# Kernel tuning notes

Hardware: AMD Instinct MI355X
Metric: run time of the kernel (lower is better)

The kernel has to match this reference:

```python
import jax, jax.numpy as jnp
import numpy as np

BATCH, N_NODES, FEAT = 32, 511, 512
N_EDGES = N_NODES - 1
N_ITERS = 9  # balanced binary tree height + 1


def setup_inputs():
    key = jax.random.key(0)
    ks = jax.random.split(key, 10)
    # balanced binary tree: node p has children 2p+1, 2p+2; leaves get order 0
    depth = np.floor(np.log2(np.arange(N_NODES) + 1)).astype(np.int32)
    order = (N_ITERS - 1 - depth).astype(np.int32)
    parents = np.repeat(np.arange((N_NODES - 1) // 2), 2).astype(np.int32)
    children = np.arange(1, N_NODES, dtype=np.int32)
    adj = np.stack([children, parents], axis=1)  # rows: [child, parent]
    eorder = order[parents]
    start = np.arange(N_NODES, dtype=np.int32)
    end = np.minimum(start + 3, N_NODES - 1).astype(np.int32)
    fin = np.stack([start, end], axis=1)
    tile = lambda a: jnp.tile(jnp.asarray(a)[None], (BATCH,) + (1,) * a.ndim)
    s = 1.0 / np.sqrt(FEAT)
    s2 = 1.0 / np.sqrt(2 * FEAT)
    return dict(
        features=jax.random.normal(ks[0], (BATCH, N_NODES, FEAT), jnp.float32),
        node_order=tile(order),
        adjacency_list=tile(adj),
        edge_order=tile(eorder),
        finlist=tile(fin),
        eh=jax.random.normal(ks[1], (BATCH, 2 * FEAT), jnp.float32),
        W_learnnode=jax.random.normal(ks[2], (FEAT, 2 * FEAT), jnp.float32) * s2,
        W_learntype_forw=jax.random.normal(ks[3], (FEAT, 2 * FEAT), jnp.float32) * s2,
        W_U_iou=jax.random.normal(ks[4], (3 * FEAT, FEAT), jnp.float32) * s,
        W_U_fe_iou=jax.random.normal(ks[5], (3 * FEAT, FEAT), jnp.float32) * s,
        b_U_fe_iou=jax.random.normal(ks[6], (3 * FEAT,), jnp.float32) * 0.01,
        W_U_f=jax.random.normal(ks[7], (FEAT, FEAT), jnp.float32) * s,
        W_U_fe_f=jax.random.normal(ks[8], (FEAT, FEAT), jnp.float32) * s,
        b_U_fe_f=jax.random.normal(ks[9], (FEAT,), jnp.float32) * 0.01,
    )


def _tree(feat, node_order, adj, edge_order, finlist, e_node, e_forw,
          W_U_iou, W_U_fe_iou, b_U_fe_iou, W_U_f, W_U_fe_f, b_U_fe_f):
    N, F = feat.shape
    j = jnp.arange(N)
    # ---- getfeature: attention-pool feature spans against e_node ----
    start, end = finlist[:, 0], finlist[:, 1]
    valid = start >= 0
    span = (j[None, :] >= start[:, None]) & (j[None, :] <= end[:, None])
    span = span | (~valid[:, None] & (j[None, :] == 0))  # keep softmax finite for dead rows
    scores = feat @ e_node  # [N]
    probs = jax.nn.softmax(jnp.where(span, scores[None, :], -jnp.inf), axis=-1)
    feat2 = jnp.where(valid[:, None], probs @ feat, 0.0)  # trainmyfeature
    numofnode = valid.sum()
    # ---- level-synchronous child-sum TreeLSTM ----
    child, parent = adj[:, 0], adj[:, 1]
    fe_iou = feat2 @ W_U_fe_iou.T + b_U_fe_iou          # U_fe_iou(features), all nodes
    fe_f = feat2[parent] @ W_U_fe_f.T + b_U_fe_f        # U_fe_f(features[parent]), all edges
    h = jnp.zeros((N, F), feat.dtype)
    c = jnp.zeros((N, F), feat.dtype)
    for n in range(N_ITERS):
        nm = (node_order == n)[:, None]
        if n == 0:
            iou = fe_iou
            c_sum = 0.0
        else:
            em = (edge_order == n).astype(feat.dtype)[:, None]
            ch, cc = h[child], c[child]
            h_sum = jnp.zeros((N, F), feat.dtype).at[parent].add(ch * em)
            iou = h_sum @ W_U_iou.T + fe_iou
            f = jax.nn.sigmoid(ch @ W_U_f.T + fe_f)
            c_sum = jnp.zeros((N, F), feat.dtype).at[parent].add(f * cc * em)
        i_g, o_g, u_g = jnp.split(iou, 3, axis=1)
        c_new = jax.nn.sigmoid(i_g) * jax.nn.relu(u_g) + c_sum
        h_new = jax.nn.sigmoid(o_g) * jnp.tanh(c_new)
        c = jnp.where(nm, c_new, c)
        h = jnp.where(nm, h_new, h)
    # ---- getfinalout: attention-pool h[0:numofnode] against e_forw ----
    root_mask = j < numofnode
    s = jax.nn.softmax(jnp.where(root_mask, (h * e_forw).sum(-1), -jnp.inf))
    return (s[:, None] * h).sum(0)


def reference(features, node_order, adjacency_list, edge_order, finlist, eh,
              W_learnnode, W_learntype_forw, W_U_iou, W_U_fe_iou, b_U_fe_iou,
              W_U_f, W_U_fe_f, b_U_fe_f):
    e_node = eh @ W_learnnode.T          # learnnode(eh)
    e_forw = eh @ W_learntype_forw.T     # learntype_forw(eh)
    return jax.vmap(_tree, in_axes=(0,) * 7 + (None,) * 6)(
        features, node_order, adjacency_list, edge_order, finlist, e_node, e_forw,
        W_U_iou, W_U_fe_iou, b_U_fe_iou, W_U_f, W_U_fe_f, b_U_fe_f)
```

## Files before the change

### kernel.cpp

```cpp
#include <hip/hip_runtime.h>
#include <hip/hip_bf16.h>

#define BATCH 32
#define NN 511
#define FEAT 512
#define NFEAT ((long)32*NN*FEAT)

typedef _Float16 half8 __attribute__((ext_vector_type(8)));
typedef float f32x4 __attribute__((ext_vector_type(4)));

__device__ __forceinline__ float bf2f(unsigned short u){
  union { unsigned int i; float f; } v; v.i = ((unsigned int)u) << 16; return v.f;
}
__device__ __forceinline__ float sigm(float x){ return 1.0f/(1.0f+expf(-x)); }
__device__ __forceinline__ float ldf(const void* p, long i, int f32){
  return f32 ? ((const float*)p)[i] : bf2f(((const unsigned short*)p)[i]);
}
__device__ __forceinline__ void gload_lds16(const _Float16* g, _Float16* l){
  __builtin_amdgcn_global_load_lds(
      (const __attribute__((address_space(1))) unsigned int*)g,
      (__attribute__((address_space(3))) unsigned int*)l, 16, 0, 0);
}

__global__ void detect_kernel(const unsigned short* __restrict__ p, int* __restrict__ flag){
  __shared__ int cnt;
  if (threadIdx.x == 0) cnt = 0;
  __syncthreads();
  int local = 0;
  for (int i = threadIdx.x; i < 4096; i += 256){
    unsigned short u = p[2*i];
    int e = (u >> 7) & 0xFF;
    if (u != 0 && e >= 117 && e <= 133) local++;
  }
  atomicAdd(&cnt, local);
  __syncthreads();
  if (threadIdx.x == 0) *flag = (cnt > 2048) ? 0 : 1;
}

__global__ void cvt_all(
    const void* __restrict__ feat, const void* __restrict__ Wiou,
    const void* __restrict__ Wfeiou, const void* __restrict__ Wf,
    const void* __restrict__ Wfef, const void* __restrict__ eh,
    const void* __restrict__ Wln, const void* __restrict__ Wlf,
    const void* __restrict__ biou, const void* __restrict__ bfv,
    _Float16* __restrict__ feat_h, _Float16* __restrict__ Wiou_h,
    _Float16* __restrict__ Wfeiou_h, _Float16* __restrict__ Wf_h,
    _Float16* __restrict__ Wfef_h, _Float16* __restrict__ eh_h,
    _Float16* __restrict__ Wln_h, _Float16* __restrict__ Wlf_h,
    float* __restrict__ biou_f, float* __restrict__ bf_f,
    const int* __restrict__ flag)
{
  long g = ((long)blockIdx.x*256 + threadIdx.x)*8;
  int f32 = *flag;
  const long S1 = NFEAT;
  const long S2 = S1 + 786432;
  const long S3 = S2 + 786432;
  const long S4 = S3 + 262144;
  const long S5 = S4 + 262144;
  const long S6 = S5 + 32768;
  const long S7 = S6 + 524288;
  const long S8 = S7 + 524288;
  const long S9 = S8 + 1536;
  const long SA = S9 + 512;
  if (g >= SA) return;
  if (g >= S9){
    long o = g - S9;
    for (int q = 0; q < 8; q++) bf_f[o+q] = ldf(bfv, o+q, f32);
    return;
  }
  if (g >= S8){
    long o = g - S8;
    for (int q = 0; q < 8; q++) biou_f[o+q] = ldf(biou, o+q, f32);
    return;
  }
  const void* src; _Float16* dst; long off;
  if      (g < S1){ src=feat;   dst=feat_h;   off=g; }
  else if (g < S2){ src=Wiou;   dst=Wiou_h;   off=g-S1; }
  else if (g < S3){ src=Wfeiou; dst=Wfeiou_h; off=g-S2; }
  else if (g < S4){ src=Wf;     dst=Wf_h;     off=g-S3; }
  else if (g < S5){ src=Wfef;   dst=Wfef_h;   off=g-S4; }
  else if (g < S6){ src=eh;     dst=eh_h;     off=g-S5; }
  else if (g < S7){ src=Wln;    dst=Wln_h;    off=g-S6; }
  else            { src=Wlf;    dst=Wlf_h;    off=g-S7; }
  #pragma unroll
  for (int q = 0; q < 8; q++) dst[off+q] = (_Float16)ldf(src, off+q, f32);
}

__global__ __launch_bounds__(64) void e_mfma(
    const _Float16* __restrict__ eh,
    const _Float16* __restrict__ Wn,
    const _Float16* __restrict__ Wf,
    float* __restrict__ e_node, float* __restrict__ e_forw)
{
  int lane = threadIdx.x;
  int m = lane & 15, quad = lane >> 4;
  int n = blockIdx.x*16 + m;
  const _Float16* wrow = (n < 512) ? (Wn + (long)n*1024) : (Wf + (long)(n-512)*1024);
  f32x4 acc[2] = {};
  for (int ks = 0; ks < 32; ks++){
    int kk = ks*32 + quad*8;
    half8 bfr = *(const half8*)(wrow + kk);
    #pragma unroll
    for (int i = 0; i < 2; i++){
      half8 afr = *(const half8*)(eh + (long)(i*16 + m)*1024 + kk);
      acc[i] = __builtin_amdgcn_mfma_f32_16x16x32_f16(afr, bfr, acc[i], 0, 0, 0);
    }
  }
  float* dst = (n < 512) ? e_node : e_forw;
  int col = (n < 512) ? n : (n - 512);
  #pragma unroll
  for (int i = 0; i < 2; i++)
    #pragma unroll
    for (int reg = 0; reg < 4; reg++){
      int b = i*16 + quad*4 + reg;
      dst[b*FEAT + col] = acc[i][reg];
    }
}

__global__ __launch_bounds__(64) void feat2_kernel(
    const _Float16* __restrict__ feat,
    const int* __restrict__ finlist,
    const float* __restrict__ e_node,
    _Float16* __restrict__ feat2){
  int i = blockIdx.x, b = blockIdx.y, lane = threadIdx.x;
  int s0 = finlist[(b*NN+i)*2+0];
  int e0 = finlist[(b*NN+i)*2+1];
  s0 = min(max(s0, 0), NN-1);
  e0 = min(max(e0, s0), NN-1);
  int w = min(e0 - s0 + 1, 4);

  const _Float16* base = feat + ((long)b*NN + s0)*FEAT + lane*8;
  half8 v[4];
  #pragma unroll
  for (int q = 0; q < 4; q++){
    if (q < w) v[q] = *(const half8*)(base + (long)q*FEAT);
    else       v[q] = half8{};
  }
  const float* ep = e_node + b*FEAT + lane*8;
  f32x4 ev0 = *(const f32x4*)ep;
  f32x4 ev1 = *(const f32x4*)(ep+4);
  float en[8] = {ev0[0],ev0[1],ev0[2],ev0[3],ev1[0],ev1[1],ev1[2],ev1[3]};

  float s[4];
  #pragma unroll
  for (int q = 0; q < 4; q++){
    float acc = 0.f;
    #pragma unroll
    for (int j = 0; j < 8; j++) acc += (float)v[q][j]*en[j];
    s[q] = acc;
  }
  #pragma unroll
  for (int q = 0; q < 4; q++)
    #pragma unroll
    for (int off = 1; off < 64; off <<= 1)
      s[q] += __shfl_xor(s[q], off, 64);

  float mx = -1e30f;
  #pragma unroll
  for (int q = 0; q < 4; q++){
    if (q >= w) s[q] = -1e30f;
    mx = fmaxf(mx, s[q]);
  }
  float p[4]; float den = 0.f;
  #pragma unroll
  for (int q = 0; q < 4; q++){ p[q] = (q < w) ? expf(s[q]-mx) : 0.f; den += p[q]; }
  float inv = 1.f/den;

  half8 o;
  #pragma unroll
  for (int j = 0; j < 8; j++){
    float acc = 0.f;
    #pragma unroll
    for (int q = 0; q < 4; q++) acc += p[q]*(float)v[q][j];
    o[j] = (_Float16)(acc*inv);
  }
  *(half8*)(feat2 + ((long)b*NN + i)*FEAT + lane*8) = o;
}

__global__ __launch_bounds__(256) void fe_gemm(
    const _Float16* __restrict__ feat2,
    const _Float16* __restrict__ Wfeiou, const _Float16* __restrict__ Wfef,
    const float* __restrict__ biou, const float* __restrict__ bf,
    _Float16* __restrict__ fe_iou, _Float16* __restrict__ fe_f)
{
  __shared__ _Float16 Abuf[2][128*64];
  __shared__ _Float16 Bbuf[2][64*64];
  const int MT = 32*NN;
  int tid = threadIdx.x;
  int wv = tid >> 6, lane = tid & 63;
  int m = lane & 15, quad = lane >> 4;
  int cg = blockIdx.y;
  int rowbase = blockIdx.x*128;
  int which = (cg < 24) ? 0 : 1;
  int colbase = which ? (cg-24)*64 : cg*64;
  const _Float16* W = which ? Wfef : Wfeiou;

  const _Float16* gA[4];
  {
    #pragma unroll
    for (int t = 0; t < 4; t++){
      int c = wv*64 + lane + t*256;
      int rt = c >> 3, kc = c & 7;
      int r = rowbase + rt; if (r >= MT) r = MT - 1;
      int bb = r / NN, node = r - bb*NN;
      int srcn = which ? ((node >= 1) ? ((node-1)>>1) : 0) : node;
      gA[t] = feat2 + ((long)bb*NN + srcn)*FEAT + ((kc ^ (rt & 7))<<3);
    }
  }
  const _Float16* gB[2];
  {
    #pragma unroll
    for (int t = 0; t < 2; t++){
      int c = wv*64 + lane + t*256;
      int rt = c >> 3, kc = c & 7;
      gB[t] = W + (long)(colbase + rt)*FEAT + ((kc ^ (rt & 7))<<3);
    }
  }

  int aoff[2][2], boff[4][2];
  #pragma unroll
  for (int i = 0; i < 2; i++)
    #pragma unroll
    for (int ks = 0; ks < 2; ks++){
      int rt = wv*32 + i*16 + m;
      aoff[i][ks] = rt*128 + (((ks*4 + quad) ^ (rt & 7))<<4);
    }
  #pragma unroll
  for (int j = 0; j < 4; j++)
    #pragma unroll
    for (int ks = 0; ks < 2; ks++){
      int rt = j*16 + m;
      boff[j][ks] = rt*128 + (((ks*4 + quad) ^ (rt & 7))<<4);
    }

  f32x4 acc[2][4] = {};

  #pragma unroll
  for (int t = 0; t < 4; t++)
    gload_lds16(gA[t], &Abuf[0][(wv*64 + t*256)*8]);
  #pragma unroll
  for (int t = 0; t < 2; t++)
    gload_lds16(gB[t], &Bbuf[0][(wv*64 + t*256)*8]);

  for (int it = 0; it < 8; ++it){
    int cur = it & 1;
    __syncthreads();
    if (it < 7){
      int kk = (it+1)*64;
      #pragma unroll
      for (int t = 0; t < 4; t++)
        gload_lds16(gA[t] + kk, &Abuf[cur^1][(wv*64 + t*256)*8]);
      #pragma unroll
      for (int t = 0; t < 2; t++)
        gload_lds16(gB[t] + kk, &Bbuf[cur^1][(wv*64 + t*256)*8]);
    }
    const char* Ab_ = (const char*)&Abuf[cur][0];
    const char* Bb_ = (const char*)&Bbuf[cur][0];
    #pragma unroll
    for (int ks = 0; ks < 2; ks++){
      half8 a0 = *(const half8*)(Ab_ + aoff[0][ks]);
      half8 a1 = *(const half8*)(Ab_ + aoff[1][ks]);
      #pragma unroll
      for (int j = 0; j < 4; j++){
        half8 bfr = *(const half8*)(Bb_ + boff[j][ks]);
        acc[0][j] = __builtin_amdgcn_mfma_f32_16x16x32_f16(a0, bfr, acc[0][j], 0, 0, 0);
        acc[1][j] = __builtin_amdgcn_mfma_f32_16x16x32_f16(a1, bfr, acc[1][j], 0, 0, 0);
      }
    }
  }
  __syncthreads();

  const float* bias = which ? bf : biou;
  float bs[4];
  #pragma unroll
  for (int j = 0; j < 4; j++) bs[j] = bias[colbase + j*16 + m];

  _Float16* sl = &Abuf[0][wv*16*72];
  int lr = lane >> 2;
  int lc = (lane & 3) * 16;
  #pragma unroll
  for (int i = 0; i < 2; i++){
    #pragma unroll
    for (int j = 0; j < 4; j++)
      #pragma unroll
      for (int reg = 0; reg < 4; reg++)
        sl[(quad*4+reg)*72 + j*16 + m] = (_Float16)(acc[i][j][reg] + bs[j]);
    half8 o0 = *(const half8*)&sl[lr*72 + lc];
    half8 o1 = *(const half8*)&sl[lr*72 + lc + 8];
    int r = rowbase + wv*32 + i*16 + lr;
    if (r < MT){
      int b = r / NN, node = r - b*NN;
      if (which == 0){
        _Float16* dst = fe_iou + ((long)b*NN + node)*1536 + colbase + lc;
        *(half8*)dst = o0; *(half8*)(dst+8) = o1;
      } else if (node >= 1){
        _Float16* dst = fe_f + ((long)b*NN + node)*FEAT + colbase + lc;
        *(half8*)dst = o0; *(half8*)(dst+8) = o1;
      }
    }
  }
}

__global__ __launch_bounds__(256) void gemm_level_staged(
    int P, int lp,
    const _Float16* __restrict__ hbuf, const _Float16* __restrict__ hsum,
    const _Float16* __restrict__ Wiou, const _Float16* __restrict__ Wf,
    _Float16* __restrict__ fe_iou, _Float16* __restrict__ fe_f)
{
  __shared__ _Float16 Abuf[2][128*64];
  __shared__ _Float16 Bbuf[2][64*64];
  int Mtot = P << 5;
  int tid = threadIdx.x;
  int wv = tid >> 6, lane = tid & 63;
  int m = lane & 15, quad = lane >> 4;
  int cg = blockIdx.y;
  int rowbase = blockIdx.x*128;
  int p0 = P - 1, c0 = 2*P - 1;
  int which, colbase;
  if (cg < 24)      { which = 0; colbase = cg*64; }
  else if (cg < 32) { which = 1; colbase = (cg-24)*64; }
  else              { which = 2; colbase = (cg-32)*64; }
  const _Float16* W = (which == 0) ? Wiou : Wf;

  const _Float16* gA[4];
  {
    #pragma unroll
    for (int t = 0; t < 4; t++){
      int c = wv*64 + lane + t*256;
      int rt = c >> 3, kc = c & 7;
      int r = rowbase + rt; if (r >= Mtot) r = Mtot - 1;
      int bb = r >> lp, p = r & (P-1);
      const _Float16* base;
      if (which == 0) base = hsum + ((long)bb*128 + p)*FEAT;
      else            base = hbuf + ((long)bb*NN + c0 + 2*p + (which==2))*FEAT;
      gA[t] = base + ((kc ^ (rt & 7))<<3);
    }
  }
  const _Float16* gB[2];
  {
    #pragma unroll
    for (int t = 0; t < 2; t++){
      int c = wv*64 + lane + t*256;
      int rt = c >> 3, kc = c & 7;
      gB[t] = W + (long)(colbase + rt)*FEAT + ((kc ^ (rt & 7))<<3);
    }
  }

  int aoff[2][2], boff[4][2];
  #pragma unroll
  for (int i = 0; i < 2; i++)
    #pragma unroll
    for (int ks = 0; ks < 2; ks++){
      int rt = wv*32 + i*16 + m;
      aoff[i][ks] = rt*128 + (((ks*4 + quad) ^ (rt & 7))<<4);
    }
  #pragma unroll
  for (int j = 0; j < 4; j++)
    #pragma unroll
    for (int ks = 0; ks < 2; ks++){
      int rt = j*16 + m;
      boff[j][ks] = rt*128 + (((ks*4 + quad) ^ (rt & 7))<<4);
    }

  f32x4 acc[2][4] = {};

  #pragma unroll
  for (int t = 0; t < 4; t++)
    gload_lds16(gA[t], &Abuf[0][(wv*64 + t*256)*8]);
  #pragma unroll
  for (int t = 0; t < 2; t++)
    gload_lds16(gB[t], &Bbuf[0][(wv*64 + t*256)*8]);

  for (int it = 0; it < 8; ++it){
    int cur = it & 1;
    __syncthreads();
    if (it < 7){
      int kk = (it+1)*64;
      #pragma unroll
      for (int t = 0; t < 4; t++)
        gload_lds16(gA[t] + kk, &Abuf[cur^1][(wv*64 + t*256)*8]);
      #pragma unroll
      for (int t = 0; t < 2; t++)
        gload_lds16(gB[t] + kk, &Bbuf[cur^1][(wv*64 + t*256)*8]);
    }
    const char* Ab_ = (const char*)&Abuf[cur][0];
    const char* Bb_ = (const char*)&Bbuf[cur][0];
    #pragma unroll
    for (int ks = 0; ks < 2; ks++){
      half8 a0 = *(const half8*)(Ab_ + aoff[0][ks]);
      half8 a1 = *(const half8*)(Ab_ + aoff[1][ks]);
      #pragma unroll
      for (int j = 0; j < 4; j++){
        half8 bfr = *(const half8*)(Bb_ + boff[j][ks]);
        acc[0][j] = __builtin_amdgcn_mfma_f32_16x16x32_f16(a0, bfr, acc[0][j], 0, 0, 0);
        acc[1][j] = __builtin_amdgcn_mfma_f32_16x16x32_f16(a1, bfr, acc[1][j], 0, 0, 0);
      }
    }
  }
  __syncthreads();

  float* fsl = (float*)((char*)&Abuf[0][0] + wv*(16*68*4));
  int lr = lane >> 2;
  int lc = (lane & 3) * 16;
  #pragma unroll
  for (int i = 0; i < 2; i++){
    #pragma unroll
    for (int j = 0; j < 4; j++)
      #pragma unroll
      for (int reg = 0; reg < 4; reg++)
        fsl[(quad*4+reg)*68 + j*16 + m] = acc[i][j][reg];
    f32x4 a0 = *(const f32x4*)&fsl[lr*68 + lc];
    f32x4 a1 = *(const f32x4*)&fsl[lr*68 + lc + 4];
    f32x4 a2 = *(const f32x4*)&fsl[lr*68 + lc + 8];
    f32x4 a3 = *(const f32x4*)&fsl[lr*68 + lc + 12];
    int r = rowbase + wv*32 + i*16 + lr;
    if (r < Mtot){
      int b = r >> lp, p = r & (P-1);
      _Float16* dst;
      if (which == 0) dst = fe_iou + ((long)b*NN + p0 + p)*1536 + colbase + lc;
      else            dst = fe_f  + ((long)b*NN + c0 + 2*p + (which-1))*FEAT + colbase + lc;
      half8 f0 = *(const half8*)dst;
      half8 f1 = *(const half8*)(dst+8);
      half8 o0, o1;
      #pragma unroll
      for (int q = 0; q < 4; q++){
        o0[q]   = (_Float16)(a0[q] + (float)f0[q]);
        o0[q+4] = (_Float16)(a1[q] + (float)f0[q+4]);
        o1[q]   = (_Float16)(a2[q] + (float)f1[q]);
        o1[q+4] = (_Float16)(a3[q] + (float)f1[q+4]);
      }
      *(half8*)dst = o0; *(half8*)(dst+8) = o1;
    }
  }
}

__global__ __launch_bounds__(64) void gemm_level_h(
    int P, int lp,
    const _Float16* __restrict__ hbuf,
    const _Float16* __restrict__ Wiou, const _Float16* __restrict__ Wf,
    _Float16* __restrict__ fe_iou, _Float16* __restrict__ fe_f)
{
  __shared__ float ldsf[16*64];
  int lane = threadIdx.x;
  int m = lane & 15, quad = lane >> 4;
  int cg = blockIdx.y;
  int Mtot = P << 5;
  int rowbase = blockIdx.x*64;
  if (rowbase >= Mtot) return;
  int p0 = P - 1, c0 = 2*P - 1;

  int which, colbase;
  if (cg < 24)      { which = 0; colbase = cg*64; }
  else if (cg < 32) { which = 1; colbase = (cg-24)*64; }
  else              { which = 2; colbase = (cg-32)*64; }

  const _Float16* W = (which == 0) ? Wiou : Wf;
  bool dual = (which == 0);

  f32x4 acc[4][4] = {};
  const _Float16* ap[4];
  const _Float16* wp[4];
  #pragma unroll
  for (int i = 0; i < 4; i++){
    int r = rowbase + i*16 + m;
    if (r >= Mtot) r = Mtot - 1;
    int b = r >> lp, p = r & (P-1);
    int node = c0 + 2*p + ((which == 2) ? 1 : 0);
    ap[i] = hbuf + ((long)b*NN + node)*FEAT + quad*8;
    wp[i] = W + (long)(colbase + i*16 + m)*FEAT + quad*8;
  }

  half8 Ab[3][4], A2b[3][4], Bb[3][4];
  #pragma unroll
  for (int s = 0; s < 2; s++){
    long kk = (long)s*32;
    #pragma unroll
    for (int i = 0; i < 4; i++){
      Ab[s][i] = *(const half8*)(ap[i] + kk);
      if (dual) A2b[s][i] = *(const half8*)(ap[i] + FEAT + kk);
      Bb[s][i] = *(const half8*)(wp[i] + kk);
    }
  }
  #pragma unroll
  for (int ks = 0; ks < 16; ++ks){
    int cur = ks % 3;
    if (ks + 2 < 16){
      int nxt = (ks + 2) % 3;
      long kk = (long)(ks + 2)*32;
      #pragma unroll
      for (int i = 0; i < 4; i++){
        Ab[nxt][i] = *(const half8*)(ap[i] + kk);
        if (dual) A2b[nxt][i] = *(const half8*)(ap[i] + FEAT + kk);
        Bb[nxt][i] = *(const half8*)(wp[i] + kk);
      }
    }
    half8 av[4];
    #pragma unroll
    for (int i = 0; i < 4; i++){
      av[i] = Ab[cur][i];
      if (dual) av[i] = av[i] + A2b[cur][i];
    }
    #pragma unroll
    for (int i = 0; i < 4; i++)
      #pragma unroll
      for (int j = 0; j < 4; j++)
        acc[i][j] = __builtin_amdgcn_mfma_f32_16x16x32_f16(av[i], Bb[cur][j], acc[i][j], 0, 0, 0);
  }

  int lr = lane >> 2;
  int lc = (lane & 3) * 16;
  #pragma unroll
  for (int i = 0; i < 4; i++){
    #pragma unroll
    for (int j = 0; j < 4; j++)
      #pragma unroll
      for (int reg = 0; reg < 4; reg++)
        ldsf[(quad*4+reg)*64 + j*16 + m] = acc[i][j][reg];
    __syncthreads();
    f32x4 a0 = *(const f32x4*)&ldsf[lr*64 + lc];
    f32x4 a1 = *(const f32x4*)&ldsf[lr*64 + lc + 4];
    f32x4 a2 = *(const f32x4*)&ldsf[lr*64 + lc + 8];
    f32x4 a3 = *(const f32x4*)&ldsf[lr*64 + lc + 12];
    int r = rowbase + i*16 + lr;
    if (r < Mtot){
      int b = r >> lp, p = r & (P-1);
      _Float16* dst;
      if (which == 0) dst = fe_iou + ((long)b*NN + p0 + p)*1536 + colbase + lc;
      else            dst = fe_f  + ((long)b*NN + c0 + 2*p + (which-1))*FEAT + colbase + lc;
      half8 f0 = *(const half8*)dst;
      half8 f1 = *(const half8*)(dst+8);
      half8 o0, o1;
      #pragma unroll
      for (int q = 0; q < 4; q++){
        o0[q]   = (_Float16)(a0[q] + (float)f0[q]);
        o0[q+4] = (_Float16)(a1[q] + (float)f0[q+4]);
        o1[q]   = (_Float16)(a2[q] + (float)f1[q]);
        o1[q+4] = (_Float16)(a3[q] + (float)f1[q+4]);
      }
      *(half8*)dst = o0; *(half8*)(dst+8) = o1;
    }
    __syncthreads();
  }
}

__global__ void pw_leaf(const _Float16* __restrict__ fe_iou, float* __restrict__ c,
                        _Float16* __restrict__ h, _Float16* __restrict__ hsum){
  int r2 = blockIdx.x, b = blockIdx.y, t = threadIdx.x;
  int l0 = 255 + 2*r2;
  const _Float16* row0 = fe_iou + ((long)b*NN + l0)*1536;
  const _Float16* row1 = row0 + 1536;
  long off0 = ((long)b*NN + l0)*FEAT;
  long off1 = off0 + FEAT;
  long so = ((long)b*128 + r2)*FEAT;
  #pragma unroll
  for (int e = 0; e < 2; e++){
    int f = t + e*256;
    float cn0 = sigm((float)row0[f])*fmaxf((float)row0[2*FEAT+f], 0.f);
    _Float16 hn0 = (_Float16)(sigm((float)row0[FEAT+f])*tanhf(cn0));
    float cn1 = sigm((float)row1[f])*fmaxf((float)row1[2*FEAT+f], 0.f);
    _Float16 hn1 = (_Float16)(sigm((float)row1[FEAT+f])*tanhf(cn1));
    c[off0+f] = cn0; h[off0+f] = hn0;
    c[off1+f] = cn1; h[off1+f] = hn1;
    hsum[so+f] = hn0 + hn1;
  }
}

__global__ void pw_level(const _Float16* __restrict__ fe_iou, const _Float16* __restrict__ fe_f,
                         float* __restrict__ c, _Float16* __restrict__ h,
                         _Float16* __restrict__ hsum,
                         int P, int p0, int c0){
  int r2 = blockIdx.x, b = blockIdx.y, t = threadIdx.x;
  int pr0 = 2*r2, pr1 = 2*r2 + 1;
  bool has1 = (pr1 < P);
  const _Float16* row0 = fe_iou + ((long)b*NN + p0 + pr0)*1536;
  const _Float16* fl0 = fe_f + ((long)b*NN + c0 + 2*pr0)*FEAT;
  long cl0 = ((long)b*NN + c0 + 2*pr0)*FEAT;
  long po0 = ((long)b*NN + p0 + pr0)*FEAT;
  long so = ((long)b*128 + r2)*FEAT;
  #pragma unroll
  for (int e = 0; e < 2; e++){
    int f = t + e*256;
    float cs0 = sigm((float)fl0[f])*c[cl0+f] + sigm((float)fl0[FEAT+f])*c[cl0+FEAT+f];
    float cn0 = sigm((float)row0[f])*fmaxf((float)row0[2*FEAT+f], 0.f) + cs0;
    _Float16 hn0 = (_Float16)(sigm((float)row0[FEAT+f])*tanhf(cn0));
    c[po0+f] = cn0; h[po0+f] = hn0;
    if (has1){
      const _Float16* row1 = row0 + 1536;
      const _Float16* fl1 = fl0 + 2*FEAT;
      long cl1 = cl0 + 2*FEAT;
      float cs1 = sigm((float)fl1[f])*c[cl1+f] + sigm((float)fl1[FEAT+f])*c[cl1+FEAT+f];
      float cn1 = sigm((float)row1[f])*fmaxf((float)row1[2*FEAT+f], 0.f) + cs1;
      _Float16 hn1 = (_Float16)(sigm((float)row1[FEAT+f])*tanhf(cn1));
      c[po0+FEAT+f] = cn1; h[po0+FEAT+f] = hn1;
      hsum[so+f] = hn0 + hn1;
    }
  }
}

__global__ void logits_kernel(const _Float16* __restrict__ h,
                              const float* __restrict__ e_forw,
                              float* __restrict__ logits){
  int b = blockIdx.y;
  int wave = threadIdx.x >> 6, lane = threadIdx.x & 63;
  int i = blockIdx.x*4 + wave;
  if (i >= NN) return;
  half8 hv = *(const half8*)(h + ((long)b*NN+i)*FEAT + lane*8);
  const float* ef = e_forw + b*FEAT + lane*8;
  float s = 0.f;
  #pragma unroll
  for (int q = 0; q < 8; q++) s += (float)hv[q]*ef[q];
  #pragma unroll
  for (int off = 32; off > 0; off >>= 1) s += __shfl_down(s, off, 64);
  if (lane == 0) logits[b*NN+i] = s;
}

__global__ void out_kernel(const _Float16* __restrict__ h,
                           const float* __restrict__ logits,
                           float* __restrict__ out){
  __shared__ float sprob[NN+1];
  __shared__ float red[128];
  int b = blockIdx.x, yc = blockIdx.y, t = threadIdx.x;
  float mx = -1e30f;
  for (int i = t; i < NN; i += 128) mx = fmaxf(mx, logits[b*NN+i]);
  red[t] = mx; __syncthreads();
  for (int s = 64; s > 0; s >>= 1){ if (t < s) red[t] = fmaxf(red[t], red[t+s]); __syncthreads(); }
  mx = red[0]; __syncthreads();
  float sum = 0.f;
  for (int i = t; i < NN; i += 128){ float p = expf(logits[b*NN+i]-mx); sprob[i] = p; sum += p; }
  red[t] = sum; __syncthreads();
  for (int s = 64; s > 0; s >>= 1){ if (t < s) red[t] += red[t+s]; __syncthreads(); }
  float inv = 1.f/red[0];
  __syncthreads();
  int f = yc*128 + t;
  float acc = 0.f;
  for (int i = 0; i < NN; i++) acc += sprob[i]*(float)h[((long)b*NN+i)*FEAT+f];
  out[b*FEAT+f] = acc*inv;
}

extern "C" void kernel_launch(void* const* d_in, const int* in_sizes, int n_in,
                              void* d_out, int out_size, void* d_ws, size_t ws_size,
                              hipStream_t stream){
  (void)in_sizes; (void)n_in; (void)out_size; (void)ws_size;
  const void* feat_raw   = d_in[0];
  const int*  finlist    = (const int*)d_in[4];
  const void* eh_raw     = d_in[5];
  const void* Wln_raw    = d_in[6];
  const void* Wlf_raw    = d_in[7];
  const void* Wiou_raw   = d_in[8];
  const void* Wfeiou_raw = d_in[9];
  const void* bfeiou_raw = d_in[10];
  const void* Wf_raw     = d_in[11];
  const void* Wfef_raw   = d_in[12];
  const void* bfef_raw   = d_in[13];

  char* ws = (char*)d_ws;
  size_t off = 0;
  auto alloc = [&](size_t bytes)->char*{
    char* p = ws + off; off += (bytes + 255) & ~(size_t)255; return p;
  };
  int*      flag     = (int*)alloc(256);
  _Float16* feat_h   = (_Float16*)alloc((size_t)NFEAT*2);
  _Float16* Wiou_h   = (_Float16*)alloc((size_t)1536*512*2);
  _Float16* Wfeiou_h = (_Float16*)alloc((size_t)1536*512*2);
  _Float16* Wf_h     = (_Float16*)alloc((size_t)512*512*2);
  _Float16* Wfef_h   = (_Float16*)alloc((size_t)512*512*2);
  _Float16* eh_h     = (_Float16*)alloc((size_t)32*1024*2);
  _Float16* Wln_h    = (_Float16*)alloc((size_t)512*1024*2);
  _Float16* Wlf_h    = (_Float16*)alloc((size_t)512*1024*2);
  float*    bfeiou_f = (float*)alloc((size_t)1536*4);
  float*    bfef_f   = (float*)alloc((size_t)512*4);
  float*    e_node   = (float*)alloc((size_t)32*512*4);
  float*    e_forw   = (float*)alloc((size_t)32*512*4);
  _Float16* feat2    = (_Float16*)alloc((size_t)NFEAT*2);
  _Float16* h_half   = (_Float16*)alloc((size_t)NFEAT*2);
  float*    c_buf    = (float*)alloc((size_t)NFEAT*4);
  _Float16* fe_iou   = (_Float16*)alloc((size_t)32*NN*1536*2);
  _Float16* hsum     = (_Float16*)alloc((size_t)32*128*512*2);
  float*    logits   = (float*)alloc((size_t)32*NN*4);
  _Float16* fe_f     = feat_h;

  detect_kernel<<<dim3(1), 256, 0, stream>>>((const unsigned short*)feat_raw, flag);

  cvt_all<<<dim3(5641), 256, 0, stream>>>(
      feat_raw, Wiou_raw, Wfeiou_raw, Wf_raw, Wfef_raw, eh_raw, Wln_raw, Wlf_raw,
      bfeiou_raw, bfef_raw,
      feat_h, Wiou_h, Wfeiou_h, Wf_h, Wfef_h, eh_h, Wln_h, Wlf_h,
      bfeiou_f, bfef_f, flag);

  e_mfma<<<dim3(64), 64, 0, stream>>>(eh_h, Wln_h, Wlf_h, e_node, e_forw);
  feat2_kernel<<<dim3(NN,32), 64, 0, stream>>>(feat_h, finlist, e_node, feat2);

  fe_gemm<<<dim3(128, 32), 256, 0, stream>>>(
      feat2, Wfeiou_h, Wfef_h, bfeiou_f, bfef_f, fe_iou, fe_f);

  pw_leaf<<<dim3(128,32), 256, 0, stream>>>(fe_iou, c_buf, h_half, hsum);

  for (int n = 1; n <= 8; n++){
    int P = 1 << (8-n);
    int lp = 8 - n;
    int p0 = P - 1, c0 = 2*P - 1;
    if (P >= 32){
      int rt = (32*P + 127)/128;
      gemm_level_staged<<<dim3(rt, 40), 256, 0, stream>>>(P, lp,
          h_half, hsum, Wiou_h, Wf_h, fe_iou, fe_f);
    } else {
      int gy = (32*P + 63)/64;
      gemm_level_h<<<dim3(gy, 40), 64, 0, stream>>>(P, lp,
          h_half, Wiou_h, Wf_h, fe_iou, fe_f);
    }
    pw_level<<<dim3((P+1)/2,32), 256, 0, stream>>>(fe_iou, fe_f, c_buf, h_half, hsum, P, p0, c0);
  }

  logits_kernel<<<dim3(128,32), 256, 0, stream>>>(h_half, e_forw, logits);
  out_kernel<<<dim3(32,4), 128, 0, stream>>>(h_half, logits, (float*)d_out);
}
```

Baseline: 394.8 us.

## Fuse small upper tree levels into one persistent per-batch kernel

Replaces the per-level GEMM and pointwise launches for levels with 16 or fewer parents with a single kernel. It runs one 1024-thread block per batch element and iterates all remaining levels with block-wide barriers. This removes many small launches and their inter-kernel gaps at the narrow top of the tree. In exchange only 32 blocks run, weights are re-read per block without LDS staging, and outputs are written with scalar half stores.

After: 825.3 us. +109.1%, slower.

```diff
diff --git a/kernel.cpp b/kernel.cpp
--- a/kernel.cpp
+++ b/kernel.cpp
@@ -434,111 +434,98 @@
   }
 }
 
-__global__ __launch_bounds__(64) void gemm_level_h(
-    int P, int lp,
-    const _Float16* __restrict__ hbuf,
+__global__ __launch_bounds__(1024) void tail_levels(
     const _Float16* __restrict__ Wiou, const _Float16* __restrict__ Wf,
-    _Float16* __restrict__ fe_iou, _Float16* __restrict__ fe_f)
+    _Float16* __restrict__ fe_iou, _Float16* __restrict__ fe_f,
+    float* __restrict__ c, _Float16* __restrict__ h,
+    _Float16* __restrict__ hsum)
 {
-  __shared__ float ldsf[16*64];
-  int lane = threadIdx.x;
+  int b = blockIdx.x;
+  int tid = threadIdx.x;
+  int wv = tid >> 6, lane = tid & 63;
   int m = lane & 15, quad = lane >> 4;
-  int cg = blockIdx.y;
-  int Mtot = P << 5;
-  int rowbase = blockIdx.x*64;
-  if (rowbase >= Mtot) return;
-  int p0 = P - 1, c0 = 2*P - 1;
-
-  int which, colbase;
-  if (cg < 24)      { which = 0; colbase = cg*64; }
-  else if (cg < 32) { which = 1; colbase = (cg-24)*64; }
-  else              { which = 2; colbase = (cg-32)*64; }
-
-  const _Float16* W = (which == 0) ? Wiou : Wf;
-  bool dual = (which == 0);
-
-  f32x4 acc[4][4] = {};
-  const _Float16* ap[4];
-  const _Float16* wp[4];
-  #pragma unroll
-  for (int i = 0; i < 4; i++){
-    int r = rowbase + i*16 + m;
-    if (r >= Mtot) r = Mtot - 1;
-    int b = r >> lp, p = r & (P-1);
-    int node = c0 + 2*p + ((which == 2) ? 1 : 0);
-    ap[i] = hbuf + ((long)b*NN + node)*FEAT + quad*8;
-    wp[i] = W + (long)(colbase + i*16 + m)*FEAT + quad*8;
-  }
-
-  half8 Ab[3][4], A2b[3][4], Bb[3][4];
-  #pragma unroll
-  for (int s = 0; s < 2; s++){
-    long kk = (long)s*32;
-    #pragma unroll
-    for (int i = 0; i < 4; i++){
-      Ab[s][i] = *(const half8*)(ap[i] + kk);
-      if (dual) A2b[s][i] = *(const half8*)(ap[i] + FEAT + kk);
-      Bb[s][i] = *(const half8*)(wp[i] + kk);
-    }
-  }
-  #pragma unroll
-  for (int ks = 0; ks < 16; ++ks){
-    int cur = ks % 3;
-    if (ks + 2 < 16){
-      int nxt = (ks + 2) % 3;
-      long kk = (long)(ks + 2)*32;
-      #pragma unroll
-      for (int i = 0; i < 4; i++){
-        Ab[nxt][i] = *(const half8*)(ap[i] + kk);
-        if (dual) A2b[nxt][i] = *(const half8*)(ap[i] + FEAT + kk);
-        Bb[nxt][i] = *(const half8*)(wp[i] + kk);
+
+  for (int P = 16; P >= 1; P >>= 1){
+    int p0 = P - 1, c0 = 2*P - 1;
+    for (int t = wv; t < 40; t += 16){
+      int which, colbase;
+      if (t < 24)      { which = 0; colbase = t*64; }
+      else if (t < 32) { which = 1; colbase = (t-24)*64; }
+      else             { which = 2; colbase = (t-32)*64; }
+      const _Float16* W = (which == 0) ? Wiou : Wf;
+      int pm = (m < P) ? m : (P-1);
+      const _Float16* arow;
+      if (which == 0) arow = hsum + ((long)b*128 + pm)*FEAT;
+      else            arow = h + ((long)b*NN + c0 + 2*pm + ((which==2)?1:0))*FEAT;
+      f32x4 acc[4] = {};
+      for (int ks = 0; ks < 16; ks++){
+        half8 av = *(const half8*)(arow + ks*32 + quad*8);
+        #pragma unroll
+        for (int j = 0; j < 4; j++){
+          half8 bv = *(const half8*)(W + (long)(colbase + j*16 + m)*FEAT + ks*32 + quad*8);
+          acc[j] = __builtin_amdgcn_mfma_f32_16x16x32_f16(av, bv, acc[j], 0, 0, 0);
+        }
       }
-    }
-    half8 av[4];
-    #pragma unroll
-    for (int i = 0; i < 4; i++){
-      av[i] = Ab[cur][i];
-      if (dual) av[i] = av[i] + A2b[cur][i];
-    }
-    #pragma unroll
-    for (int i = 0; i < 4; i++)
       #pragma unroll
       for (int j = 0; j < 4; j++)
-        acc[i][j] = __builtin_amdgcn_mfma_f32_16x16x32_f16(av[i], Bb[cur][j], acc[i][j], 0, 0, 0);
-  }
-
-  int lr = lane >> 2;
-  int lc = (lane & 3) * 16;
-  #pragma unroll
-  for (int i = 0; i < 4; i++){
-    #pragma unroll
-    for (int j = 0; j < 4; j++)
-      #pragma unroll
-      for (int reg = 0; reg < 4; reg++)
-        ldsf[(quad*4+reg)*64 + j*16 + m] = acc[i][j][reg];
+        #pragma unroll
+        for (int reg = 0; reg < 4; reg++){
+          int pr = quad*4 + reg;
+          if (pr < P){
+            int n = colbase + j*16 + m;
+            _Float16* dst;
+            if (which == 0) dst = fe_iou + ((long)b*NN + p0 + pr)*1536 + n;
+            else            dst = fe_f  + ((long)b*NN + c0 + 2*pr + (which-1))*FEAT + n;
+            *dst = (_Float16)(acc[j][reg] + (float)*dst);
+          }
+        }
+    }
+    __threadfence_block();
     __syncthreads();
-    f32x4 a0 = *(const f32x4*)&ldsf[lr*64 + lc];
-    f32x4 a1 = *(const f32x4*)&ldsf[lr*64 + lc + 4];
-    f32x4 a2 = *(const f32x4*)&ldsf[lr*64 + lc + 8];
-    f32x4 a3 = *(const f32x4*)&ldsf[lr*64 + lc + 12];
-    int r = rowbase + i*16 + lr;
-    if (r < Mtot){
-      int b = r >> lp, p = r & (P-1);
-      _Float16* dst;
-      if (which == 0) dst = fe_iou + ((long)b*NN + p0 + p)*1536 + colbase + lc;
-      else            dst = fe_f  + ((long)b*NN + c0 + 2*p + (which-1))*FEAT + colbase + lc;
-      half8 f0 = *(const half8*)dst;
-      half8 f1 = *(const half8*)(dst+8);
-      half8 o0, o1;
-      #pragma unroll
-      for (int q = 0; q < 4; q++){
-        o0[q]   = (_Float16)(a0[q] + (float)f0[q]);
-        o0[q+4] = (_Float16)(a1[q] + (float)f0[q+4]);
-        o1[q]   = (_Float16)(a2[q] + (float)f1[q]);
-        o1[q+4] = (_Float16)(a3[q] + (float)f1[q+4]);
+    if (P > 1){
+      int base = tid*8;
+      int r2 = base >> 9, f0 = base & 511;
+      if (r2 < (P>>1)){
+        const _Float16* row0 = fe_iou + ((long)b*NN + p0 + 2*r2)*1536;
+        const _Float16* row1 = row0 + 1536;
+        const _Float16* fl0 = fe_f + ((long)b*NN + c0 + 4*r2)*FEAT;
+        long cl0 = ((long)b*NN + c0 + 4*r2)*FEAT;
+        long po0 = ((long)b*NN + p0 + 2*r2)*FEAT;
+        long so = ((long)b*128 + r2)*FEAT;
+        #pragma unroll
+        for (int q = 0; q < 8; q++){
+          int f = f0 + q;
+          float cs0 = sigm((float)fl0[f])*c[cl0+f] + sigm((float)fl0[FEAT+f])*c[cl0+FEAT+f];
+          float cn0 = sigm((float)row0[f])*fmaxf((float)row0[2*FEAT+f], 0.f) + cs0;
+          _Float16 hn0 = (_Float16)(sigm((float)row0[FEAT+f])*tanhf(cn0));
+          const _Float16* fl1 = fl0 + 2*FEAT;
+          long cl1 = cl0 + 2*FEAT;
+          float cs1 = sigm((float)fl1[f])*c[cl1+f] + sigm((float)fl1[FEAT+f])*c[cl1+FEAT+f];
+          float cn1 = sigm((float)row1[f])*fmaxf((float)row1[2*FEAT+f], 0.f) + cs1;
+          _Float16 hn1 = (_Float16)(sigm((float)row1[FEAT+f])*tanhf(cn1));
+          c[po0+f] = cn0; h[po0+f] = hn0;
+          c[po0+FEAT+f] = cn1; h[po0+FEAT+f] = hn1;
+          hsum[so+f] = hn0 + hn1;
+        }
       }
-      *(half8*)dst = o0; *(half8*)(dst+8) = o1;
-    }
+    } else {
+      int base = tid*8;
+      if (base < 512){
+        const _Float16* row = fe_iou + ((long)b*NN)*1536;
+        const _Float16* fl = fe_f + ((long)b*NN + 1)*FEAT;
+        long cl = ((long)b*NN + 1)*FEAT;
+        long po = ((long)b*NN)*FEAT;
+        #pragma unroll
+        for (int q = 0; q < 8; q++){
+          int f = base + q;
+          float cs = sigm((float)fl[f])*c[cl+f] + sigm((float)fl[FEAT+f])*c[cl+FEAT+f];
+          float cn = sigm((float)row[f])*fmaxf((float)row[2*FEAT+f], 0.f) + cs;
+          float hn = sigm((float)row[FEAT+f])*tanhf(cn);
+          c[po+f] = cn; h[po+f] = (_Float16)hn;
+        }
+      }
+    }
+    __threadfence_block();
     __syncthreads();
   }
 }
@@ -695,21 +682,18 @@
 
   pw_leaf<<<dim3(128,32), 256, 0, stream>>>(fe_iou, c_buf, h_half, hsum);
 
-  for (int n = 1; n <= 8; n++){
+  for (int n = 1; n <= 3; n++){
     int P = 1 << (8-n);
     int lp = 8 - n;
     int p0 = P - 1, c0 = 2*P - 1;
-    if (P >= 32){
-      int rt = (32*P + 127)/128;
-      gemm_level_staged<<<dim3(rt, 40), 256, 0, stream>>>(P, lp,
-          h_half, hsum, Wiou_h, Wf_h, fe_iou, fe_f);
-    } else {
-      int gy = (32*P + 63)/64;
-      gemm_level_h<<<dim3(gy, 40), 64, 0, stream>>>(P, lp,
-          h_half, Wiou_h, Wf_h, fe_iou, fe_f);
-    }
+    int rt = (32*P + 127)/128;
+    gemm_level_staged<<<dim3(rt, 40), 256, 0, stream>>>(P, lp,
+        h_half, hsum, Wiou_h, Wf_h, fe_iou, fe_f);
     pw_level<<<dim3((P+1)/2,32), 256, 0, stream>>>(fe_iou, fe_f, c_buf, h_half, hsum, P, p0, c0);
   }
+
+  tail_levels<<<dim3(32), 1024, 0, stream>>>(
+      Wiou_h, Wf_h, fe_iou, fe_f, c_buf, h_half, hsum);
 
   logits_kernel<<<dim3(128,32), 256, 0, stream>>>(h_half, e_forw, logits);
   out_kernel<<<dim3(32,4), 128, 0, stream>>>(h_half, logits, (float*)d_out);
```
